# Optimization experiments

Hardware: AMD Instinct MI355X
Metric: run time of the kernel (lower is better)

Reference implementation:

```python
import jax, jax.numpy as jnp
import numpy as np

BETA = 0.9
THR = 1.0
B, T, F, H = 64, 256, 1024, 512

# snntorch heaviside spike with ATan surrogate gradient (alpha=2.0, snntorch default)
@jax.custom_vjp
def spike_fn(u):
    return (u > 0).astype(u.dtype)

def _spike_fwd(u):
    return spike_fn(u), u

def _spike_bwd(u, g):
    alpha = 2.0
    grad = (alpha / 2.0) / (1.0 + (jnp.pi / 2.0 * alpha * u) ** 2)
    return (g * grad,)

spike_fn.defvjp(_spike_fwd, _spike_bwd)


def setup_inputs() -> dict:
    key = jax.random.key(0)
    ks = jax.random.split(key, 12)
    s = 0.05
    return {
        "f_f": jax.random.normal(ks[0], (B, T, F), dtype=jnp.float32),
        "seq_len": jnp.full((B,), T, dtype=jnp.int64),
        "Wf": jax.random.normal(ks[1], (H, F), dtype=jnp.float32) * s,
        "bf": jnp.zeros((H,), jnp.float32),
        "W1": jax.random.normal(ks[2], (H, H), dtype=jnp.float32) * s,
        "b1": jnp.zeros((H,), jnp.float32),
        "W2": jax.random.normal(ks[3], (H, H), dtype=jnp.float32) * s,
        "b2": jnp.zeros((H,), jnp.float32),
        "Mw1": jax.random.normal(ks[4], (512, H), dtype=jnp.float32) * s,
        "Mb1": jnp.zeros((512,), jnp.float32),
        "Mw2": jax.random.normal(ks[5], (32, 512), dtype=jnp.float32) * s,
        "Mb2": jnp.zeros((32,), jnp.float32),
        "Mw3": jax.random.normal(ks[6], (1, 32), dtype=jnp.float32) * s,
        "Mb3": jnp.zeros((1,), jnp.float32),
    }


def _forward(f_f, Wf, bf, W1, b1, W2, b2, Mw1, Mb1, Mw2, Mb2, Mw3, Mb3):
    h = f_f @ Wf.T + bf            # [B,T,H] fc_f
    x1 = h @ W1.T + b1             # layer-1 linear drive precomputed (state-independent)

    def step(carry, x1_t):
        m1, m2 = carry
        # snntorch Leaky (subtract reset): reset from previous mem's spike
        r1 = spike_fn(m1 - THR)
        m1 = BETA * m1 + x1_t - r1 * THR
        s1 = spike_fn(m1 - THR)
        x2 = s1 @ W2.T + b2        # layer-2 linear on spikes (dropout=identity, eval)
        r2 = spike_fn(m2 - THR)
        m2 = BETA * m2 + x2 - r2 * THR
        s2 = spike_fn(m2 - THR)
        return (m1, m2), s2

    init = (jnp.zeros((B, H), h.dtype), jnp.zeros((B, H), h.dtype))
    _, spk = jax.lax.scan(step, init, jnp.swapaxes(x1, 0, 1))  # [T,B,H]
    spk = jnp.swapaxes(spk, 0, 1)                              # [B,T,H]

    z = jax.nn.relu(spk @ Mw1.T + Mb1)
    z = z @ Mw2.T + Mb2
    logits = jax.nn.sigmoid((z @ Mw3.T + Mb3).squeeze(-1))     # [B,T]

    # filter: top-(seq_len//16 + 1) mean per clip; seq_len == T for all clips
    k = T // 16 + 1
    topv, _ = jax.lax.top_k(logits, k)
    return jnp.mean(topv, axis=-1)                             # [B]


def reference(f_f, seq_len, Wf, bf, W1, b1, W2, b2, Mw1, Mb1, Mw2, Mb2, Mw3, Mb3):
    return _forward(f_f, Wf, bf, W1, b1, W2, b2, Mw1, Mb1, Mw2, Mb2, Mw3, Mb3)
```

## Files before the change

kernel.cpp:

```cpp
#include <hip/hip_runtime.h>
#include <math.h>

#define BETA 0.9f
#define THR 1.0f

constexpr int B_ = 64, T_ = 256, F_ = 1024, H_ = 512;
constexpr int M_ = B_ * T_;

typedef float f32x4 __attribute__((ext_vector_type(4)));
typedef short short8 __attribute__((ext_vector_type(8)));
typedef _Float16 half8 __attribute__((ext_vector_type(8)));
typedef unsigned short us4 __attribute__((ext_vector_type(4)));
typedef unsigned short ushort_t;

static __device__ __forceinline__ unsigned short f2bf(float x) {
    unsigned b = __builtin_bit_cast(unsigned, x);
    unsigned r = (b + 0x7FFFu + ((b >> 16) & 1u)) >> 16;
    return (unsigned short)r;
}
static __device__ __forceinline__ float bf2f(unsigned short u) {
    unsigned v = ((unsigned)u) << 16;
    return __builtin_bit_cast(float, v);
}
static __device__ __forceinline__ unsigned short f2h(float x) {
    _Float16 h = (_Float16)x;
    return __builtin_bit_cast(unsigned short, h);
}
static __device__ __forceinline__ float h2f(unsigned short u) {
    return (float)__builtin_bit_cast(_Float16, u);
}
static __device__ __forceinline__ int swz(int r) {
    return ((r >> 2) & 3) ^ (r & 3);
}

#define GLDS(srcp, dstp)                                                      \
    __builtin_amdgcn_global_load_lds(                                         \
        (const __attribute__((address_space(1))) unsigned int*)(srcp),        \
        (__attribute__((address_space(3))) unsigned int*)(dstp), 16, 0, 0)

__global__ __launch_bounds__(256) void gemm_scan(
    const ushort_t* __restrict__ Ap, const ushort_t* __restrict__ Bp,
    const float* __restrict__ bias, ushort_t* __restrict__ Sout, int K) {
    constexpr int BUF = 20480;
    __shared__ ushort_t lds[2 * BUF];

    const int tid = threadIdx.x;
    const int w = tid >> 6, l = tid & 63;
    const int flat = blockIdx.y * gridDim.x + blockIdx.x;
    const int clip = ((flat >> 6) << 3) | (flat & 7);
    const int strip = (flat >> 3) & 7;
    const int n0 = strip * 64;
    const int m0 = clip * 256;

    f32x4 acc[4][4];
#pragma unroll
    for (int mi = 0; mi < 4; ++mi)
#pragma unroll
        for (int ni = 0; ni < 4; ++ni) acc[mi][ni] = (f32x4){0.f, 0.f, 0.f, 0.f};

    const int c0 = l >> 4;
    const int schunk = (l & 7) ^ ((l >> 3) & 7);

    auto stage = [&](int buf, int k0) {
#pragma unroll
        for (int j = 0; j < 10; ++j) {
            const int seg = w * 10 + j;
            if (seg < 32) {
                const int r = seg * 8 + (l >> 3);
                GLDS(Ap + (size_t)(m0 + r) * K + k0 + schunk * 8,
                     &lds[buf + seg * 512]);
            } else {
                const int r = (seg - 32) * 8 + (l >> 3);
                GLDS(Bp + (size_t)(n0 + r) * K + k0 + schunk * 8,
                     &lds[buf + 16384 + (seg - 32) * 512]);
            }
        }
    };

    const int nt = K / 64;
    stage(0, 0);
    for (int t = 0; t < nt; ++t) {
        const int cur = (t & 1) * BUF;
        const int nxt = BUF - cur;
        __syncthreads();
        if (t + 1 < nt) stage(nxt, (t + 1) * 64);

#pragma unroll
        for (int kh = 0; kh < 2; ++kh) {
            half8 aa[4], bb[4];
            const int q = kh * 4 + c0;
#pragma unroll
            for (int mi = 0; mi < 4; ++mi) {
                const int r = w * 64 + mi * 16 + (l & 15);
                const int off = cur + r * 64 + ((q ^ (l & 7)) * 8);
                aa[mi] = __builtin_bit_cast(half8, *(const short8*)&lds[off]);
            }
#pragma unroll
            for (int ni = 0; ni < 4; ++ni) {
                const int r = ni * 16 + (l & 15);
                const int off = cur + 16384 + r * 64 + ((q ^ (l & 7)) * 8);
                bb[ni] = __builtin_bit_cast(half8, *(const short8*)&lds[off]);
            }
#pragma unroll
            for (int mi = 0; mi < 4; ++mi)
#pragma unroll
                for (int ni = 0; ni < 4; ++ni)
                    acc[mi][ni] = __builtin_amdgcn_mfma_f32_16x16x32_f16(
                        aa[mi], bb[ni], acc[mi][ni], 0, 0, 0);
        }
    }

    float bv[4];
#pragma unroll
    for (int ni = 0; ni < 4; ++ni) bv[ni] = bias[n0 + ni * 16 + (l & 15)];
#pragma unroll
    for (int mi = 0; mi < 4; ++mi) {
        const int t0 = w * 64 + mi * 16 + ((l >> 4) << 2);
#pragma unroll
        for (int ni = 0; ni < 4; ++ni) {
            const int h = ni * 16 + (l & 15);
#pragma unroll
            for (int r = 0; r < 4; ++r)
                lds[(t0 + r) * 66 + h] = f2h(acc[mi][ni][r] + bv[ni]);
        }
    }
    __syncthreads();

    if (tid < 64) {
        const int h = tid;
        ushort_t* sp = Sout + (size_t)m0 * 512 + n0 + h;
        float m = 0.f;
#pragma unroll 4
        for (int t = 0; t < T_; ++t) {
            const float xv = h2f(lds[t * 66 + h]);
            const float r = (m - THR > 0.f) ? THR : 0.f;
            m = BETA * m + xv - r;
            sp[(size_t)t * 512] = (m - THR > 0.f) ? (ushort_t)0x3C00 : (ushort_t)0;
        }
    }
}

__global__ __launch_bounds__(256) void gemm_mil(
    const ushort_t* __restrict__ Ap, const ushort_t* __restrict__ Bp,
    const float* __restrict__ bias, const float* __restrict__ Uv,
    float* __restrict__ part, int N, int K) {
    constexpr int BUF = 16384;
    __shared__ ushort_t lds[2 * BUF];

    const int tid = threadIdx.x;
    const int w = tid >> 6, l = tid & 63;
    const int flat = blockIdx.y * gridDim.x + blockIdx.x;
    const int mt = ((flat >> 5) << 3) | (flat & 7);
    const int st = (flat >> 3) & 3;
    const int n0 = st * 128;
    const int m0 = mt * 128;
    const int wr = w >> 1, wc = w & 1;

    f32x4 acc[4][4];
#pragma unroll
    for (int mi = 0; mi < 4; ++mi)
#pragma unroll
        for (int ni = 0; ni < 4; ++ni) acc[mi][ni] = (f32x4){0.f, 0.f, 0.f, 0.f};

    const int c0 = l >> 4;
    const int schunk = (l & 7) ^ ((l >> 3) & 7);

    auto stage = [&](int buf, int k0) {
#pragma unroll
        for (int j = 0; j < 8; ++j) {
            const int g = w * 8 + j;
            const int seg = g & 15;
            const int r = seg * 8 + (l >> 3);
            const ushort_t* pl = (g < 16) ? Ap : Bp;
            const int rb = (g < 16) ? m0 : n0;
            GLDS(pl + (size_t)(rb + r) * K + k0 + schunk * 8,
                 &lds[buf + g * 512]);
        }
    };

    const int nt = K / 64;
    stage(0, 0);
    for (int t = 0; t < nt; ++t) {
        const int cur = (t & 1) * BUF;
        const int nxt = BUF - cur;
        __syncthreads();
        if (t + 1 < nt) stage(nxt, (t + 1) * 64);

#pragma unroll
        for (int kh = 0; kh < 2; ++kh) {
            half8 aa[4], bb[4];
            const int q = kh * 4 + c0;
#pragma unroll
            for (int mi = 0; mi < 4; ++mi) {
                const int r = wr * 64 + mi * 16 + (l & 15);
                const int off = cur + r * 64 + ((q ^ (l & 7)) * 8);
                aa[mi] = __builtin_bit_cast(half8, *(const short8*)&lds[off]);
            }
#pragma unroll
            for (int ni = 0; ni < 4; ++ni) {
                const int r = wc * 64 + ni * 16 + (l & 15);
                const int off = cur + 8192 + r * 64 + ((q ^ (l & 7)) * 8);
                bb[ni] = __builtin_bit_cast(half8, *(const short8*)&lds[off]);
            }
#pragma unroll
            for (int mi = 0; mi < 4; ++mi)
#pragma unroll
                for (int ni = 0; ni < 4; ++ni)
                    acc[mi][ni] = __builtin_amdgcn_mfma_f32_16x16x32_f16(
                        aa[mi], bb[ni], acc[mi][ni], 0, 0, 0);
        }
    }

    float bv[4], uc[4];
#pragma unroll
    for (int ni = 0; ni < 4; ++ni) {
        const int col = n0 + wc * 64 + ni * 16 + (l & 15);
        bv[ni] = bias[col];
        uc[ni] = Uv[col];
    }
    const int strip = (n0 >> 6) + wc;
#pragma unroll
    for (int mi = 0; mi < 4; ++mi) {
        float p[4];
#pragma unroll
        for (int r = 0; r < 4; ++r) {
            float s = 0.f;
#pragma unroll
            for (int ni = 0; ni < 4; ++ni)
                s += fmaxf(acc[mi][ni][r] + bv[ni], 0.f) * uc[ni];
            p[r] = s;
        }
#pragma unroll
        for (int off = 1; off <= 8; off <<= 1)
#pragma unroll
            for (int r = 0; r < 4; ++r) p[r] += __shfl_xor(p[r], off);
        if ((l & 15) == 0) {
            const int row0 = m0 + wr * 64 + mi * 16 + ((l >> 4) << 2);
#pragma unroll
            for (int r = 0; r < 4; ++r)
                part[(size_t)strip * M_ + row0 + r] = p[r];
        }
    }
}

__global__ __launch_bounds__(256) void gemm_bf16_wc(
    const ushort_t* __restrict__ Ah, const ushort_t* __restrict__ Al,
    const ushort_t* __restrict__ Bh, const ushort_t* __restrict__ Bl,
    ushort_t* __restrict__ Cout, int N, int K) {
    __shared__ ushort_t lds[4 * 4096];

    const int tid = threadIdx.x;
    const int w = tid >> 6, l = tid & 63;
    const int nwg = gridDim.x * gridDim.y;
    const int flat = blockIdx.y * gridDim.x + blockIdx.x;
    const int wg = (flat & 7) * (nwg >> 3) + (flat >> 3);
    const int n0 = (wg % gridDim.x) * 128;
    const int m0 = (wg / gridDim.x) * 128;
    const int wr = w >> 1, wc = w & 1;

    f32x4 acc[4][4];
#pragma unroll
    for (int mi = 0; mi < 4; ++mi)
#pragma unroll
        for (int ni = 0; ni < 4; ++ni) acc[mi][ni] = (f32x4){0.f, 0.f, 0.f, 0.f};

    const int c0 = l >> 4;
    for (int k0 = 0; k0 < K; k0 += 32) {
        __syncthreads();
#pragma unroll
        for (int j = 0; j < 8; ++j) {
            const int g = w * 8 + j;
            const int p = g >> 3, seg = g & 7;
            const int r = seg * 16 + (l >> 2);
            const int ch = (l & 3) ^ swz(r);
            const ushort_t* pl = (p == 0) ? Ah : (p == 1) ? Al : (p == 2) ? Bh : Bl;
            const int rb = (p < 2) ? m0 : n0;
            GLDS(pl + (size_t)(rb + r) * K + k0 + ch * 8,
                 &lds[p * 4096 + seg * 512]);
        }
        __syncthreads();

        short8 ah[4], al[4], bh[4], bl[4];
#pragma unroll
        for (int mi = 0; mi < 4; ++mi) {
            const int r = wr * 64 + mi * 16 + (l & 15);
            const int off = r * 32 + ((c0 ^ swz(r)) * 8);
            ah[mi] = *(const short8*)&lds[off];
            al[mi] = *(const short8*)&lds[4096 + off];
        }
#pragma unroll
        for (int ni = 0; ni < 4; ++ni) {
            const int r = wc * 64 + ni * 16 + (l & 15);
            const int off = r * 32 + ((c0 ^ swz(r)) * 8);
            bh[ni] = *(const short8*)&lds[8192 + off];
            bl[ni] = *(const short8*)&lds[12288 + off];
        }
#pragma unroll
        for (int mi = 0; mi < 4; ++mi)
#pragma unroll
            for (int ni = 0; ni < 4; ++ni) {
                acc[mi][ni] = __builtin_amdgcn_mfma_f32_16x16x32_bf16(
                    ah[mi], bh[ni], acc[mi][ni], 0, 0, 0);
                acc[mi][ni] = __builtin_amdgcn_mfma_f32_16x16x32_bf16(
                    ah[mi], bl[ni], acc[mi][ni], 0, 0, 0);
                acc[mi][ni] = __builtin_amdgcn_mfma_f32_16x16x32_bf16(
                    al[mi], bh[ni], acc[mi][ni], 0, 0, 0);
            }
    }

#pragma unroll
    for (int ni = 0; ni < 4; ++ni) {
        const int col = n0 + wc * 64 + ni * 16 + (l & 15);
#pragma unroll
        for (int mi = 0; mi < 4; ++mi) {
            const int row0 = m0 + wr * 64 + mi * 16 + ((l >> 4) << 2);
#pragma unroll
            for (int r = 0; r < 4; ++r)
                Cout[(size_t)(row0 + r) * N + col] = f2h(acc[mi][ni][r]);
        }
    }
}

__global__ __launch_bounds__(256) void prep_small(
    const float* __restrict__ W1, const float* __restrict__ W2,
    const float* __restrict__ Mw1, const float* __restrict__ bfv,
    const float* __restrict__ b1, const float* __restrict__ Mw2,
    const float* __restrict__ Mb2, const float* __restrict__ Mw3,
    const float* __restrict__ Mb3, const float* __restrict__ Wf,
    const float* __restrict__ f_f, ushort_t* __restrict__ w1h,
    ushort_t* __restrict__ w1l, ushort_t* __restrict__ w2f,
    ushort_t* __restrict__ m1f, float* __restrict__ bc,
    float* __restrict__ uc, ushort_t* __restrict__ wfTh,
    ushort_t* __restrict__ wfTl, ushort_t* __restrict__ ffh) {
    __shared__ float tile[32][33];
    const int blk = blockIdx.x;
    const int tid = threadIdx.x;
    if (blk < 256) {
        const int i = blk * 256 + tid;
        f32x4 v = ((const f32x4*)W1)[i];
        us4 h, ll;
#pragma unroll
        for (int e = 0; e < 4; ++e) {
            const unsigned short hb = f2bf(v[e]);
            h[e] = hb;
            ll[e] = f2bf(v[e] - bf2f(hb));
        }
        ((us4*)w1h)[i] = h;
        ((us4*)w1l)[i] = ll;
    } else if (blk < 512) {
        const int i = (blk - 256) * 256 + tid;
        f32x4 v = ((const f32x4*)W2)[i];
        us4 h;
#pragma unroll
        for (int e = 0; e < 4; ++e) h[e] = f2h(v[e]);
        ((us4*)w2f)[i] = h;
    } else if (blk < 768) {
        const int i = (blk - 512) * 256 + tid;
        f32x4 v = ((const f32x4*)Mw1)[i];
        us4 h;
#pragma unroll
        for (int e = 0; e < 4; ++e) h[e] = f2h(v[e]);
        ((us4*)m1f)[i] = h;
    } else if (blk < 896) {
        const int w = tid >> 6, l = tid & 63;
        const int j = (blk - 768) * 4 + w;
        const float* row = W1 + (size_t)j * 512;
        float a = 0.f;
#pragma unroll
        for (int i = 0; i < 8; ++i) a += row[l + i * 64] * bfv[l + i * 64];
#pragma unroll
        for (int off = 32; off >= 1; off >>= 1) a += __shfl_xor(a, off);
        if (l == 0) bc[j] = a + b1[j];
    } else if (blk < 898) {
        const int j = (blk - 896) * 256 + tid;
        float a = 0.f;
        for (int i = 0; i < 32; ++i) a += Mw3[i] * Mw2[(size_t)i * 512 + j];
        uc[j] = a;
        if (j == 0) {
            float c = Mb3[0];
            for (int i = 0; i < 32; ++i) c += Mw3[i] * Mb2[i];
            uc[512] = c;
        }
    } else if (blk < 1410) {
        const int idx = blk - 898;
        const int k0 = (idx & 31) * 32;
        const int i0 = (idx >> 5) * 32;
        const int tx = tid & 31;
        const int ty = tid >> 5;
#pragma unroll
        for (int e = 0; e < 4; ++e) {
            const int i = ty + e * 8;
            tile[i][tx] = Wf[(size_t)(i0 + i) * 1024 + k0 + tx];
        }
        __syncthreads();
#pragma unroll
        for (int e = 0; e < 4; ++e) {
            const int kk = ty + e * 8;
            const float v = tile[tx][kk];
            const unsigned short h = f2bf(v);
            wfTh[(size_t)(k0 + kk) * 512 + i0 + tx] = h;
            wfTl[(size_t)(k0 + kk) * 512 + i0 + tx] = f2bf(v - bf2f(h));
        }
    } else {
        constexpr int n4 = 4194304;
        const int base = (blk - 1410) * 256 + tid;
        for (int i = base; i < n4; i += 2048 * 256) {
            f32x4 v = ((const f32x4*)f_f)[i];
            us4 h;
#pragma unroll
            for (int e = 0; e < 4; ++e) h[e] = f2h(v[e]);
            ((us4*)ffh)[i] = h;
        }
    }
}

__global__ __launch_bounds__(64) void tail_topk(const float* __restrict__ part,
                                                const float* __restrict__ uc,
                                                float* __restrict__ out) {
    const int b = blockIdx.x;
    const int lane = threadIdx.x;
    const float c = uc[512];
    float v[4];
#pragma unroll
    for (int i = 0; i < 4; ++i) {
        const int row = b * T_ + lane + i * 64;
        float a = 0.f;
#pragma unroll
        for (int s = 0; s < 8; ++s) a += part[(size_t)s * M_ + row];
        v[i] = a + c;
    }
    float sum = 0.f;
    for (int iter = 0; iter < 17; ++iter) {
        float mv = v[0];
        int mslot = 0;
#pragma unroll
        for (int i = 1; i < 4; ++i)
            if (v[i] > mv) { mv = v[i]; mslot = i; }
        float bv = mv;
        int bl = lane, bs = mslot;
#pragma unroll
        for (int off = 32; off >= 1; off >>= 1) {
            const float ov = __shfl_xor(bv, off);
            const int ol = __shfl_xor(bl, off);
            const int os = __shfl_xor(bs, off);
            if (ov > bv || (ov == bv && ol < bl)) { bv = ov; bl = ol; bs = os; }
        }
        sum += 1.f / (1.f + expf(-bv));
        if (lane == bl) v[bs] = -1e30f;
    }
    if (lane == 0) out[b] = sum * (1.f / 17.f);
}

extern "C" void kernel_launch(void* const* d_in, const int* in_sizes, int n_in,
                              void* d_out, int out_size, void* d_ws, size_t ws_size,
                              hipStream_t stream) {
    const float* f_f = (const float*)d_in[0];
    const float* Wf  = (const float*)d_in[2];
    const float* bf  = (const float*)d_in[3];
    const float* W1  = (const float*)d_in[4];
    const float* b1  = (const float*)d_in[5];
    const float* W2  = (const float*)d_in[6];
    const float* b2  = (const float*)d_in[7];
    const float* Mw1 = (const float*)d_in[8];
    const float* Mb1 = (const float*)d_in[9];
    const float* Mw2 = (const float*)d_in[10];
    const float* Mb2 = (const float*)d_in[11];
    const float* Mw3 = (const float*)d_in[12];
    const float* Mb3 = (const float*)d_in[13];
    float* out = (float*)d_out;

    char* ws = (char*)d_ws;
    const size_t NEf = (size_t)M_ * F_;
    const size_t NE = (size_t)M_ * H_;
    ushort_t* ffh = (ushort_t*)ws;
    ushort_t* sbuf1 = ffh + NEf;
    ushort_t* sbuf2 = sbuf1 + NE;
    ushort_t* w1h = sbuf2 + NE;
    ushort_t* w1l = w1h + 262144;
    ushort_t* w2f = w1l + 262144;
    ushort_t* m1f = w2f + 262144;
    ushort_t* wfTh = m1f + 262144;
    ushort_t* wfTl = wfTh + 524288;
    ushort_t* wcf = wfTl + 524288;
    float* bc = (float*)(wcf + 524288);
    float* uc = bc + 512;
    float* part = uc + 513 + 63;

    const dim3 blk(256);

    prep_small<<<dim3(3458), blk, 0, stream>>>(W1, W2, Mw1, bf, b1, Mw2, Mb2,
                                               Mw3, Mb3, Wf, f_f, w1h, w1l,
                                               w2f, m1f, bc, uc, wfTh, wfTl,
                                               ffh);

    gemm_bf16_wc<<<dim3(8, 4), blk, 0, stream>>>(w1h, w1l, wfTh, wfTl, wcf,
                                                 1024, 512);
    gemm_scan<<<dim3(8, 64), blk, 0, stream>>>(ffh, wcf, bc, sbuf1, 1024);
    gemm_scan<<<dim3(8, 64), blk, 0, stream>>>(sbuf1, w2f, b2, sbuf2, 512);
    gemm_mil<<<dim3(4, 128), blk, 0, stream>>>(sbuf2, m1f, Mb1, uc, part,
                                               512, 512);
    tail_topk<<<dim3(B_), dim3(64), 0, stream>>>(part, uc, out);
}
```

Measured before the change: 119.7 us.

## Fuse f32-to-f16 input conversion into first GEMM-scan A-tile loading

Removes the separate pass in prep_small that converted the whole f_f input to fp16 in a workspace buffer. The first gemm_scan now loads fp32 rows into registers, converts them to fp16, and writes them swizzled into LDS after the MFMA loop, overlapping the next tile's load with compute. This avoids writing and rereading a 32 MB intermediate, but it costs register pressure and replaces async global-to-LDS loads with register-staged loads. Launch bounds also gain a minimum-blocks hint of 2.

```diff
diff --git a/kernel.cpp b/kernel.cpp
--- a/kernel.cpp
+++ b/kernel.cpp
@@ -11,6 +11,7 @@
 typedef short short8 __attribute__((ext_vector_type(8)));
 typedef _Float16 half8 __attribute__((ext_vector_type(8)));
 typedef unsigned short us4 __attribute__((ext_vector_type(4)));
+typedef unsigned short us8 __attribute__((ext_vector_type(8)));
 typedef unsigned short ushort_t;
 
 static __device__ __forceinline__ unsigned short f2bf(float x) {
@@ -38,8 +39,9 @@
         (const __attribute__((address_space(1))) unsigned int*)(srcp),        \
         (__attribute__((address_space(3))) unsigned int*)(dstp), 16, 0, 0)
 
-__global__ __launch_bounds__(256) void gemm_scan(
-    const ushort_t* __restrict__ Ap, const ushort_t* __restrict__ Bp,
+template <int AF32>
+__global__ __launch_bounds__(256, 2) void gemm_scan(
+    const void* __restrict__ Asrc, const ushort_t* __restrict__ Bp,
     const float* __restrict__ bias, ushort_t* __restrict__ Sout, int K) {
     constexpr int BUF = 20480;
     __shared__ ushort_t lds[2 * BUF];
@@ -61,29 +63,70 @@
     const int c0 = l >> 4;
     const int schunk = (l & 7) ^ ((l >> 3) & 7);
 
-    auto stage = [&](int buf, int k0) {
-#pragma unroll
-        for (int j = 0; j < 10; ++j) {
-            const int seg = w * 10 + j;
-            if (seg < 32) {
-                const int r = seg * 8 + (l >> 3);
-                GLDS(Ap + (size_t)(m0 + r) * K + k0 + schunk * 8,
-                     &lds[buf + seg * 512]);
-            } else {
-                const int r = (seg - 32) * 8 + (l >> 3);
-                GLDS(Bp + (size_t)(n0 + r) * K + k0 + schunk * 8,
-                     &lds[buf + 16384 + (seg - 32) * 512]);
+    f32x4 areg[8][2];
+
+    auto stageB = [&](int buf, int k0) {
+#pragma unroll
+        for (int j = 0; j < 2; ++j) {
+            const int seg = w * 2 + j;
+            const int r = seg * 8 + (l >> 3);
+            GLDS((const ushort_t*)Bp + (size_t)(n0 + r) * K + k0 + schunk * 8,
+                 &lds[buf + 16384 + seg * 512]);
+        }
+    };
+    auto stageA16 = [&](int buf, int k0) {
+#pragma unroll
+        for (int j = 0; j < 8; ++j) {
+            const int seg = w * 8 + j;
+            const int r = seg * 8 + (l >> 3);
+            GLDS((const ushort_t*)Asrc + (size_t)(m0 + r) * K + k0 + schunk * 8,
+                 &lds[buf + seg * 512]);
+        }
+    };
+    auto loadA32 = [&](int k0) {
+#pragma unroll
+        for (int j = 0; j < 8; ++j) {
+            const int r = j * 32 + w * 8 + (l >> 3);
+            const float* src =
+                (const float*)Asrc + (size_t)(m0 + r) * K + k0 + (l & 7) * 8;
+            areg[j][0] = *(const f32x4*)src;
+            areg[j][1] = *(const f32x4*)(src + 4);
+        }
+    };
+    auto writeA32 = [&](int buf) {
+#pragma unroll
+        for (int j = 0; j < 8; ++j) {
+            const int r = j * 32 + w * 8 + (l >> 3);
+            us8 hv;
+#pragma unroll
+            for (int e = 0; e < 4; ++e) {
+                hv[e] = f2h(areg[j][0][e]);
+                hv[e + 4] = f2h(areg[j][1][e]);
             }
+            const int pos = (l & 7) ^ (r & 7);
+            *(us8*)&lds[buf + r * 64 + pos * 8] = hv;
         }
     };
 
     const int nt = K / 64;
-    stage(0, 0);
+    if constexpr (AF32) {
+        loadA32(0);
+        writeA32(0);
+    } else {
+        stageA16(0, 0);
+    }
+    stageB(0, 0);
+
     for (int t = 0; t < nt; ++t) {
         const int cur = (t & 1) * BUF;
         const int nxt = BUF - cur;
         __syncthreads();
-        if (t + 1 < nt) stage(nxt, (t + 1) * 64);
+        const bool more = (t + 1 < nt);
+        if (more) {
+            if constexpr (AF32) loadA32((t + 1) * 64);
+            else stageA16(nxt, (t + 1) * 64);
+            stageB(nxt, (t + 1) * 64);
+        }
 
 #pragma unroll
         for (int kh = 0; kh < 2; ++kh) {
@@ -107,6 +150,10 @@
                 for (int ni = 0; ni < 4; ++ni)
                     acc[mi][ni] = __builtin_amdgcn_mfma_f32_16x16x32_f16(
                         aa[mi], bb[ni], acc[mi][ni], 0, 0, 0);
+        }
+
+        if constexpr (AF32) {
+            if (more) writeA32(nxt);
         }
     }
 
@@ -327,11 +374,10 @@
     const float* __restrict__ b1, const float* __restrict__ Mw2,
     const float* __restrict__ Mb2, const float* __restrict__ Mw3,
     const float* __restrict__ Mb3, const float* __restrict__ Wf,
-    const float* __restrict__ f_f, ushort_t* __restrict__ w1h,
-    ushort_t* __restrict__ w1l, ushort_t* __restrict__ w2f,
-    ushort_t* __restrict__ m1f, float* __restrict__ bc,
-    float* __restrict__ uc, ushort_t* __restrict__ wfTh,
-    ushort_t* __restrict__ wfTl, ushort_t* __restrict__ ffh) {
+    ushort_t* __restrict__ w1h, ushort_t* __restrict__ w1l,
+    ushort_t* __restrict__ w2f, ushort_t* __restrict__ m1f,
+    float* __restrict__ bc, float* __restrict__ uc,
+    ushort_t* __restrict__ wfTh, ushort_t* __restrict__ wfTl) {
     __shared__ float tile[32][33];
     const int blk = blockIdx.x;
     const int tid = threadIdx.x;
@@ -381,7 +427,7 @@
             for (int i = 0; i < 32; ++i) c += Mw3[i] * Mb2[i];
             uc[512] = c;
         }
-    } else if (blk < 1410) {
+    } else {
         const int idx = blk - 898;
         const int k0 = (idx & 31) * 32;
         const int i0 = (idx >> 5) * 32;
@@ -400,16 +446,6 @@
             const unsigned short h = f2bf(v);
             wfTh[(size_t)(k0 + kk) * 512 + i0 + tx] = h;
             wfTl[(size_t)(k0 + kk) * 512 + i0 + tx] = f2bf(v - bf2f(h));
-        }
-    } else {
-        constexpr int n4 = 4194304;
-        const int base = (blk - 1410) * 256 + tid;
-        for (int i = base; i < n4; i += 2048 * 256) {
-            f32x4 v = ((const f32x4*)f_f)[i];
-            us4 h;
-#pragma unroll
-            for (int e = 0; e < 4; ++e) h[e] = f2h(v[e]);
-            ((us4*)ffh)[i] = h;
         }
     }
 }
@@ -470,10 +506,8 @@
     float* out = (float*)d_out;
 
     char* ws = (char*)d_ws;
-    const size_t NEf = (size_t)M_ * F_;
     const size_t NE = (size_t)M_ * H_;
-    ushort_t* ffh = (ushort_t*)ws;
-    ushort_t* sbuf1 = ffh + NEf;
+    ushort_t* sbuf1 = (ushort_t*)ws;
     ushort_t* sbuf2 = sbuf1 + NE;
     ushort_t* w1h = sbuf2 + NE;
     ushort_t* w1l = w1h + 262144;
@@ -488,15 +522,14 @@
 
     const dim3 blk(256);
 
-    prep_small<<<dim3(3458), blk, 0, stream>>>(W1, W2, Mw1, bf, b1, Mw2, Mb2,
-                                               Mw3, Mb3, Wf, f_f, w1h, w1l,
-                                               w2f, m1f, bc, uc, wfTh, wfTl,
-                                               ffh);
+    prep_small<<<dim3(1410), blk, 0, stream>>>(W1, W2, Mw1, bf, b1, Mw2, Mb2,
+                                               Mw3, Mb3, Wf, w1h, w1l, w2f,
+                                               m1f, bc, uc, wfTh, wfTl);
 
     gemm_bf16_wc<<<dim3(8, 4), blk, 0, stream>>>(w1h, w1l, wfTh, wfTl, wcf,
                                                  1024, 512);
-    gemm_scan<<<dim3(8, 64), blk, 0, stream>>>(ffh, wcf, bc, sbuf1, 1024);
-    gemm_scan<<<dim3(8, 64), blk, 0, stream>>>(sbuf1, w2f, b2, sbuf2, 512);
+    gemm_scan<1><<<dim3(8, 64), blk, 0, stream>>>(f_f, wcf, bc, sbuf1, 1024);
+    gemm_scan<0><<<dim3(8, 64), blk, 0, stream>>>(sbuf1, w2f, b2, sbuf2, 512);
     gemm_mil<<<dim3(4, 128), blk, 0, stream>>>(sbuf2, m1f, Mb1, uc, part,
                                                512, 512);
     tail_topk<<<dim3(B_), dim3(64), 0, stream>>>(part, uc, out);
```

Measured after the change: 114.3 us. 1.05x faster.
